# Performance work log

Hardware: AMD Instinct MI355X
Metric: run time of the kernel (lower is better)

The kernel has to match this reference:

```python
import jax, jax.numpy as jnp
import numpy as np

N = 20000      # nodes
E = 256000     # edges
H = 8          # heads
DIN = 256      # in_dim_struct / in_dim_semantic
DH = 32        # num_hidden per head (H*DH == DIN for GT residual)
PRED = 32      # pred_dim (relation embedding dim)
REL = 16       # rel_num
NEG = 0.2      # negative_slope for GAT attention
ALPHA = 0.5    # args.fusion
NUM_LAYERS = 2


def seg_softmax(e, seg, n):
    # softmax over edges grouped by destination node; e: [E, ...], seg: [E]
    m = jax.ops.segment_max(e, seg, num_segments=n)
    ex = jnp.exp(e - m[seg])
    s = jax.ops.segment_sum(ex, seg, num_segments=n)
    return ex / (s[seg] + 1e-9)


def setup_inputs() -> dict:
    key = jax.random.key(0)
    ks = jax.random.split(key, 24)
    f32 = jnp.float32
    def rn(k, shape, scale=0.05):
        return jax.random.normal(k, shape, dtype=f32) * scale
    return {
        "feats_struct": jax.random.normal(ks[0], (N, DIN), f32),
        "feats_semantic": jax.random.normal(ks[1], (N, DIN), f32),
        "centrality": jax.random.uniform(ks[2], (N,), f32),
        # fused per-head scoring MLP (heads[0] small Sequentials batched over H)
        "Ws1": rn(ks[3], (H, DIN, DIN // 2)),
        "bs1": jnp.zeros((H, DIN // 2), f32),
        "Ws2": rn(ks[4], (H, DIN // 2)),
        "bs2": jnp.zeros((H,), f32),
        "rel_emb": rn(ks[5], (REL, PRED), 1.0),
        # SALayer params (2 layers, per-head scalar channels)
        "sa_w": rn(ks[6], (NUM_LAYERS, H), 1.0),
        "sa_al": rn(ks[7], (NUM_LAYERS, H), 1.0),
        "sa_ar": rn(ks[8], (NUM_LAYERS, H), 1.0),
        "sa_We": rn(ks[9], (NUM_LAYERS, PRED, H)),
        # GTLayer params
        "Wq": rn(ks[10], (DIN, H * DH)),
        "bq": jnp.zeros((H * DH,), f32),
        "Wk": rn(ks[11], (DIN, H * DH)),
        "bk": jnp.zeros((H * DH,), f32),
        "Wv": rn(ks[12], (DIN, H * DH)),
        "bv": jnp.zeros((H * DH,), f32),
        "We_gt": rn(ks[13], (PRED, H * DH)),
        "bn_gamma": jnp.ones((H * DH,), f32),
        "bn_beta": jnp.zeros((H * DH,), f32),
        "Wout": rn(ks[14], (H * DH, 1)),
        "bout": jnp.zeros((1,), f32),
        # centrality scale params
        "gamma": jnp.ones((1, H), f32),
        "beta": jnp.zeros((1, H), f32),
        "edge_types": jax.random.randint(ks[15], (E,), 0, REL),
        "edge_src": jax.random.randint(ks[16], (E,), 0, N),
        "edge_dst": jax.random.randint(ks[17], (E,), 0, N),
    }


def _forward(feats_struct, feats_semantic, centrality, Ws1, bs1, Ws2, bs2,
             rel_emb, sa_w, sa_al, sa_ar, sa_We, Wq, bq, Wk, bk, Wv, bv,
             We_gt, bn_gamma, bn_beta, Wout, bout, gamma, beta,
             edge_types, edge_src, edge_dst):
    n = feats_struct.shape[0]
    edge_feats = rel_emb[edge_types]                                   # [E, PRED]

    # ---- structural channel: fused per-head scoring MLPs ----
    h1 = jax.nn.relu(jnp.einsum('nd,hdk->nhk', feats_struct, Ws1) + bs1)  # [N,H,DIN/2]
    h = jnp.einsum('nhk,hk->nh', h1, Ws2) + bs2                           # [N,H]

    # ---- SALayer stack (GAT-style, per-head scalar features) ----
    for l in range(NUM_LAYERS):
        z = h * sa_w[l]                                                 # [N,H]
        e = jax.nn.leaky_relu(z[edge_src] * sa_al[l] + z[edge_dst] * sa_ar[l]
                              + edge_feats @ sa_We[l], NEG)             # [E,H]
        attn = seg_softmax(e, edge_dst, n)                              # [E,H]
        out = jax.ops.segment_sum(attn * z[edge_src], edge_dst, num_segments=n)
        h = jax.nn.elu(out + z)                                         # residual + activation
        if l != NUM_LAYERS - 1:
            h = jnp.mean(h, axis=-1, keepdims=True)
            h = jnp.tile(h, (1, H))
    logits_struct = h                                                   # [N,H]

    # ---- semantic channel: Graph Transformer layer (edge_mode='MUL') ----
    q = (feats_semantic @ Wq + bq).reshape(n, H, DH)
    k = (feats_semantic @ Wk + bk).reshape(n, H, DH)
    v = (feats_semantic @ Wv + bv).reshape(n, H, DH)
    ep = (edge_feats @ We_gt).reshape(-1, H, DH)                        # [E,H,DH]
    ke = k[edge_src] * ep                                               # MUL edge gating
    score = jnp.sum(q[edge_dst] * ke, axis=-1) / jnp.sqrt(jnp.float32(DH))  # [E,H]
    attn = seg_softmax(score, edge_dst, n)                              # [E,H]
    agg = jax.ops.segment_sum(attn[..., None] * v[edge_src], edge_dst,
                              num_segments=n).reshape(n, H * DH)
    agg = agg + feats_semantic                                          # residual (H*DH == DIN)
    mu = jnp.mean(agg, axis=0)
    var = jnp.var(agg, axis=0)
    agg = (agg - mu) / jnp.sqrt(var + 1e-5) * bn_gamma + bn_beta        # batch norm
    h_sem = jax.nn.relu(agg)
    logits_semantic = h_sem @ Wout + bout                               # [N,1]

    # ---- fusion + centrality gamma/beta scaling ----
    logits = ALPHA * logits_struct + (1.0 - ALPHA) * logits_semantic    # [N,H]
    scaled = (centrality[:, None] * gamma + beta) * logits              # [N,H]
    return jax.nn.leaky_relu(jnp.mean(scaled, axis=-1, keepdims=True), 0.01)


def reference(feats_struct, feats_semantic, centrality, Ws1, bs1, Ws2, bs2,
              rel_emb, sa_w, sa_al, sa_ar, sa_We, Wq, bq, Wk, bk, Wv, bv,
              We_gt, bn_gamma, bn_beta, Wout, bout, gamma, beta,
              edge_types, edge_src, edge_dst):
    return _forward(feats_struct, feats_semantic, centrality, Ws1, bs1, Ws2, bs2,
                    rel_emb, sa_w, sa_al, sa_ar, sa_We, Wq, bq, Wk, bk, Wv, bv,
                    We_gt, bn_gamma, bn_beta, Wout, bout, gamma, beta,
                    edge_types, edge_src, edge_dst)
```

## Files before the change

kernel.cpp:

```cpp
#include <hip/hip_runtime.h>
#include <hip/hip_bf16.h>
#include <math.h>

#define N_NODES 20000
#define N_EDGES 256000
#define LOG2E 1.4426950408889634f

typedef __attribute__((ext_vector_type(8))) __bf16 bf16x8;
typedef __attribute__((ext_vector_type(8))) unsigned short u16x8;
typedef __attribute__((ext_vector_type(4))) float f32x4;

static __device__ __forceinline__ unsigned short f2bf(float f) {
  unsigned u = __float_as_uint(f);
  unsigned r = (u + 0x7fffu + ((u >> 16) & 1u)) >> 16;
  return (unsigned short)r;
}
static __device__ __forceinline__ float b2f(unsigned short u) {
  return __uint_as_float((unsigned)u << 16);
}

__global__ __launch_bounds__(256) void k_setup(
    const float* __restrict__ rel_emb, const float* __restrict__ sa_We,
    const float* __restrict__ We_gt, const float* __restrict__ Xs,
    const float* __restrict__ Xm, const float* __restrict__ Ws1,
    const float* __restrict__ Wq, const float* __restrict__ Wk,
    const float* __restrict__ Wv, const int* __restrict__ e_dst,
    float* __restrict__ saTab, float* __restrict__ epTab,
    ushort* __restrict__ Xsb, ushort* __restrict__ Xmb,
    ushort* __restrict__ Ws1t, ushort* __restrict__ Wt,
    int* __restrict__ deg) {
  int b = blockIdx.x;
  int t = threadIdx.x;
  if (b == 0) {
    {
      int l = t >> 7, r = (t >> 3) & 15, h = t & 7;
      float acc = 0.f;
      for (int p = 0; p < 32; ++p)
        acc += rel_emb[r * 32 + p] * sa_We[l * 256 + p * 8 + h];
      saTab[t] = acc * LOG2E;
    }
    for (int r = 0; r < 16; ++r) {
      float acc = 0.f;
      for (int p = 0; p < 32; ++p)
        acc += rel_emb[r * 32 + p] * We_gt[p * 256 + t];
      epTab[r * 256 + t] = acc;
    }
  } else if (b < 5001) {
    size_t i = ((size_t)(b - 1) * 256 + t) * 4;
    float4 a = *(const float4*)(Xs + i);
    ushort4 ua = {f2bf(a.x), f2bf(a.y), f2bf(a.z), f2bf(a.w)};
    *(ushort4*)(Xsb + i) = ua;
    float4 c = *(const float4*)(Xm + i);
    ushort4 uc = {f2bf(c.x), f2bf(c.y), f2bf(c.z), f2bf(c.w)};
    *(ushort4*)(Xmb + i) = uc;
  } else if (b < 6025) {
    int lb = b - 5001;
    int h = lb >> 7, kcol = lb & 127;
    Ws1t[((size_t)h * 128 + kcol) * 256 + t] =
        f2bf(Ws1[((size_t)h * 256 + t) * 128 + kcol]);
  } else if (b < 6793) {
    int lb = b - 6025;
    int m = lb >> 8, n = lb & 255;
    const float* W = (m == 0) ? Wq : (m == 1) ? Wk : Wv;
    Wt[((size_t)m * 256 + n) * 256 + t] = f2bf(W[(size_t)t * 256 + n]);
  } else {
    int e = (b - 6793) * 256 + t;
    if (e < N_EDGES) atomicAdd(&deg[e_dst[e]], 1);
  }
}

__global__ __launch_bounds__(1024) void k_scan(const int* __restrict__ deg,
                                               int* __restrict__ rowPtr,
                                               int* __restrict__ cursor) {
  const int CH = (N_NODES + 1023) / 1024;
  int t = threadIdx.x;
  int b0 = t * CH, b1 = min(b0 + CH, N_NODES);
  int s = 0;
  for (int i = b0; i < b1; ++i) s += deg[i];
  __shared__ int part[1024];
  part[t] = s;
  __syncthreads();
  for (int off = 1; off < 1024; off <<= 1) {
    int add = (t >= off) ? part[t - off] : 0;
    __syncthreads();
    part[t] += add;
    __syncthreads();
  }
  int run = (t == 0) ? 0 : part[t - 1];
  for (int i = b0; i < b1; ++i) {
    rowPtr[i] = run;
    cursor[i] = run;
    run += deg[i];
  }
  if (t == 0) rowPtr[N_NODES] = part[1023];
}

__global__ void k_fill(const int* __restrict__ e_dst, const int* __restrict__ e_src,
                       const int* __restrict__ e_type, int* __restrict__ cursor,
                       int2* __restrict__ csrPack) {
  int e = blockIdx.x * 256 + threadIdx.x;
  if (e >= N_EDGES) return;
  int d = e_dst[e];
  int pos = atomicAdd(&cursor[d], 1);
  csrPack[pos] = make_int2(e_src[e], e_type[e]);
}

__global__ __launch_bounds__(256) void k_gemm(
    const ushort* __restrict__ Xsb, const ushort* __restrict__ Xmb,
    const ushort* __restrict__ Ws1t, const ushort* __restrict__ Wqkvt,
    const float* __restrict__ bs1, const float* __restrict__ Ws2,
    const float* __restrict__ bs2, const float* __restrict__ bq,
    const float* __restrict__ bk, const float* __restrict__ bv,
    float* __restrict__ h0, float* __restrict__ q, ushort* __restrict__ kvB) {
  __shared__ ushort Ab[128][128];
  __shared__ ushort Bb[128][128];
  int tid = threadIdx.x;
  int y = blockIdx.y;
  bool isMlp = (y < 8);
  int m = 0, half = 0;
  const ushort* Bsrc;
  const ushort* Xb;
  if (isMlp) {
    Xb = Xsb;
    Bsrc = Ws1t + (size_t)y * 128 * 256;
  } else {
    m = (y - 8) >> 1;
    half = (y - 8) & 1;
    Xb = Xmb;
    Bsrc = Wqkvt + ((size_t)m * 256 + half * 128) * 256;
  }
  int base = blockIdx.x * 128;
  int wv = tid >> 6, lane = tid & 63;
  int l15 = lane & 15, lhi = lane >> 4;
  int rs = tid >> 4;
  int cs = (tid & 15) * 8;
  f32x4 acc[2][8];
  #pragma unroll
  for (int mr = 0; mr < 2; ++mr)
    #pragma unroll
    for (int nt = 0; nt < 8; ++nt) acc[mr][nt] = (f32x4){0.f, 0.f, 0.f, 0.f};

  for (int kc = 0; kc < 2; ++kc) {
    #pragma unroll
    for (int s = 0; s < 8; ++s) {
      int r = rs + s * 16;
      int csw = cs ^ ((r & 7) << 3);
      int gr = base + r;
      u16x8 val = {0, 0, 0, 0, 0, 0, 0, 0};
      if (gr < N_NODES) val = *(const u16x8*)(Xb + (size_t)gr * 256 + kc * 128 + cs);
      *(u16x8*)&Ab[r][csw] = val;
    }
    #pragma unroll
    for (int s = 0; s < 8; ++s) {
      int r = rs + s * 16;
      int csw = cs ^ ((r & 7) << 3);
      *(u16x8*)&Bb[r][csw] = *(const u16x8*)(Bsrc + (size_t)r * 256 + kc * 128 + cs);
    }
    __syncthreads();
    int swzA = (l15 & 7) << 3;
    #pragma unroll
    for (int kk = 0; kk < 4; ++kk) {
      int col = (kk * 32 + lhi * 8);
      bf16x8 a0 = *(const bf16x8*)&Ab[wv * 32 + l15][col ^ swzA];
      bf16x8 a1 = *(const bf16x8*)&Ab[wv * 32 + 16 + l15][col ^ swzA];
      #pragma unroll
      for (int nt = 0; nt < 8; ++nt) {
        bf16x8 b = *(const bf16x8*)&Bb[nt * 16 + l15][col ^ swzA];
        acc[0][nt] = __builtin_amdgcn_mfma_f32_16x16x32_bf16(a0, b, acc[0][nt], 0, 0, 0);
        acc[1][nt] = __builtin_amdgcn_mfma_f32_16x16x32_bf16(a1, b, acc[1][nt], 0, 0, 0);
      }
    }
    __syncthreads();
  }

  if (isMlp) {
    float part[2][4] = {{0.f, 0.f, 0.f, 0.f}, {0.f, 0.f, 0.f, 0.f}};
    #pragma unroll
    for (int nt = 0; nt < 8; ++nt) {
      int c = y * 128 + nt * 16 + l15;
      float b1 = bs1[c], w2 = Ws2[c];
      #pragma unroll
      for (int mr = 0; mr < 2; ++mr)
        #pragma unroll
        for (int j = 0; j < 4; ++j)
          part[mr][j] += fmaxf(acc[mr][nt][j] + b1, 0.f) * w2;
    }
    #pragma unroll
    for (int mr = 0; mr < 2; ++mr)
      #pragma unroll
      for (int j = 0; j < 4; ++j) {
        #pragma unroll
        for (int o = 1; o < 16; o <<= 1) part[mr][j] += __shfl_xor(part[mr][j], o);
      }
    if (l15 == 0) {
      float b2 = bs2[y];
      #pragma unroll
      for (int mr = 0; mr < 2; ++mr)
        #pragma unroll
        for (int j = 0; j < 4; ++j) {
          int row = base + wv * 32 + mr * 16 + lhi * 4 + j;
          if (row < N_NODES) h0[(size_t)row * 8 + y] = part[mr][j] + b2;
        }
    }
  } else {
    const float* bias = (m == 0) ? bq : (m == 1) ? bk : bv;
    #pragma unroll
    for (int nt = 0; nt < 8; ++nt) {
      int c = half * 128 + nt * 16 + l15;
      float bc = bias[c];
      #pragma unroll
      for (int mr = 0; mr < 2; ++mr)
        #pragma unroll
        for (int j = 0; j < 4; ++j) {
          int row = base + wv * 32 + mr * 16 + lhi * 4 + j;
          if (row < N_NODES) {
            float val = acc[mr][nt][j] + bc;
            if (m == 0) q[(size_t)row * 256 + c] = val;
            else if (m == 1) kvB[(size_t)row * 512 + c] = f2bf(val);
            else kvB[(size_t)row * 512 + 256 + c] = f2bf(val);
          }
        }
    }
  }
}


__global__ __launch_bounds__(256) void k_sa(const float* __restrict__ h_in,
                                            float* __restrict__ h_out,
                                            const int* __restrict__ rowPtr,
                                            const int2* __restrict__ csrPack,
                                            const float* __restrict__ sa_w,
                                            const float* __restrict__ sa_al,
                                            const float* __restrict__ sa_ar,
                                            const float* __restrict__ saTab, int layer) {
  int node = blockIdx.x * 4 + (threadIdx.x >> 6);
  int lane = threadIdx.x & 63;
  int h = lane & 7, eslot = lane >> 3;
  float wgt = sa_w[layer * 8 + h];
  float al2 = sa_al[layer * 8 + h] * LOG2E;
  float ar2 = sa_ar[layer * 8 + h] * LOG2E;
  const float* tab = saTab + layer * 128;
  float zd = h_in[(size_t)node * 8 + h] * wgt;
  int s0 = rowPtr[node], s1 = rowPtr[node + 1];
  float m = -1e30f, lsum = 0.f, acc = 0.f;
  for (int i = s0 + eslot; i < s1; i += 8) {
    int2 p = csrPack[i];
    float zs = h_in[(size_t)p.x * 8 + h] * wgt;
    float e = zs * al2 + zd * ar2 + tab[p.y * 8 + h];
    e = (e >= 0.f) ? e : 0.2f * e;
    float nm = fmaxf(m, e);
    float scl = exp2f(m - nm);
    float pw = exp2f(e - nm);
    acc = acc * scl + pw * zs;
    lsum = lsum * scl + pw;
    m = nm;
  }
  #pragma unroll
  for (int off = 8; off < 64; off <<= 1) {
    float om = __shfl_xor(m, off);
    float ol = __shfl_xor(lsum, off);
    float oa = __shfl_xor(acc, off);
    float nm = fmaxf(m, om);
    float sl = exp2f(m - nm);
    float so = exp2f(om - nm);
    acc = acc * sl + oa * so;
    lsum = lsum * sl + ol * so;
    m = nm;
  }
  float o = acc / (lsum + 1e-9f);
  float r = o + zd;
  r = (r > 0.f) ? r : expm1f(r);
  if (layer == 0) {
    r += __shfl_xor(r, 1);
    r += __shfl_xor(r, 2);
    r += __shfl_xor(r, 4);
    r *= 0.125f;
  }
  if (eslot == 0) h_out[(size_t)node * 8 + h] = r;
}


__global__ __launch_bounds__(256) void k_gt(const float* __restrict__ q,
                                            const ushort* __restrict__ kvB,
                                            const float* __restrict__ epTab,
                                            const float* __restrict__ feats_sem,
                                            const int* __restrict__ rowPtr,
                                            const int2* __restrict__ csrPack,
                                            ushort* __restrict__ agg) {
  int node = blockIdx.x * 4 + (threadIdx.x >> 6);
  int lane = threadIdx.x & 63;
  int c0 = lane * 4;
  const float SC2 = 0.17677669529663687f * LOG2E;
  float4 qv = *(const float4*)(q + (size_t)node * 256 + c0);
  qv.x *= SC2; qv.y *= SC2; qv.z *= SC2; qv.w *= SC2;
  float4 acc = {0.f, 0.f, 0.f, 0.f};
  float m = -1e30f, lsum = 0.f;
  int s0 = rowPtr[node], s1 = rowPtr[node + 1];
  int i = s0;
  for (; i + 1 < s1; i += 2) {
    int2 eA = csrPack[i], eB = csrPack[i + 1];
    const ushort* rA = kvB + (size_t)eA.x * 512 + c0;
    const ushort* rB = kvB + (size_t)eB.x * 512 + c0;
    ushort4 kA = *(const ushort4*)rA;
    ushort4 kB4 = *(const ushort4*)rB;
    float4 epA = *(const float4*)(epTab + eA.y * 256 + c0);
    float4 epB = *(const float4*)(epTab + eB.y * 256 + c0);
    ushort4 vA = *(const ushort4*)(rA + 256);
    ushort4 vB = *(const ushort4*)(rB + 256);
    float pA = qv.x * b2f(kA.x) * epA.x + qv.y * b2f(kA.y) * epA.y +
               qv.z * b2f(kA.z) * epA.z + qv.w * b2f(kA.w) * epA.w;
    float pB = qv.x * b2f(kB4.x) * epB.x + qv.y * b2f(kB4.y) * epB.y +
               qv.z * b2f(kB4.z) * epB.z + qv.w * b2f(kB4.w) * epB.w;
    pA += __shfl_xor(pA, 1); pB += __shfl_xor(pB, 1);
    pA += __shfl_xor(pA, 2); pB += __shfl_xor(pB, 2);
    pA += __shfl_xor(pA, 4); pB += __shfl_xor(pB, 4);
    float nm = fmaxf(m, fmaxf(pA, pB));
    float scl = exp2f(m - nm);
    float wA = exp2f(pA - nm);
    float wB = exp2f(pB - nm);
    acc.x = acc.x * scl + wA * b2f(vA.x) + wB * b2f(vB.x);
    acc.y = acc.y * scl + wA * b2f(vA.y) + wB * b2f(vB.y);
    acc.z = acc.z * scl + wA * b2f(vA.z) + wB * b2f(vB.z);
    acc.w = acc.w * scl + wA * b2f(vA.w) + wB * b2f(vB.w);
    lsum = lsum * scl + wA + wB;
    m = nm;
  }
  if (i < s1) {
    int2 eA = csrPack[i];
    const ushort* rA = kvB + (size_t)eA.x * 512 + c0;
    ushort4 kv = *(const ushort4*)rA;
    float4 ep = *(const float4*)(epTab + eA.y * 256 + c0);
    ushort4 vv = *(const ushort4*)(rA + 256);
    float part = qv.x * b2f(kv.x) * ep.x + qv.y * b2f(kv.y) * ep.y +
                 qv.z * b2f(kv.z) * ep.z + qv.w * b2f(kv.w) * ep.w;
    part += __shfl_xor(part, 1);
    part += __shfl_xor(part, 2);
    part += __shfl_xor(part, 4);
    float nm = fmaxf(m, part);
    float scl = exp2f(m - nm);
    float pw = exp2f(part - nm);
    acc.x = acc.x * scl + pw * b2f(vv.x);
    acc.y = acc.y * scl + pw * b2f(vv.y);
    acc.z = acc.z * scl + pw * b2f(vv.z);
    acc.w = acc.w * scl + pw * b2f(vv.w);
    lsum = lsum * scl + pw;
    m = nm;
  }
  float inv = 1.f / (lsum + 1e-9f);
  float4 fs = *(const float4*)(feats_sem + (size_t)node * 256 + c0);
  ushort4 r;
  r.x = f2bf(acc.x * inv + fs.x);
  r.y = f2bf(acc.y * inv + fs.y);
  r.z = f2bf(acc.z * inv + fs.z);
  r.w = f2bf(acc.w * inv + fs.w);
  *(ushort4*)(agg + (size_t)node * 256 + c0) = r;
}

__global__ void k_bnstats(const ushort* __restrict__ agg, double* __restrict__ colsum,
                          double* __restrict__ colssq) {
  int t = threadIdx.x;
  int r0 = blockIdx.x * 79;
  int r1 = min(r0 + 79, N_NODES);
  double s = 0.0, qq = 0.0;
  for (int r = r0; r < r1; ++r) {
    float x = b2f(agg[(size_t)r * 256 + t]);
    s += (double)x;
    qq += (double)x * (double)x;
  }
  atomicAdd(&colsum[t], s);
  atomicAdd(&colssq[t], qq);
}

__global__ void k_bnfinal(const double* __restrict__ colsum, const double* __restrict__ colssq,
                          float* __restrict__ muArr, float* __restrict__ invArr) {
  int t = threadIdx.x;
  double mu = colsum[t] / (double)N_NODES;
  double var = colssq[t] / (double)N_NODES - mu * mu;
  muArr[t] = (float)mu;
  invArr[t] = (float)(1.0 / sqrt(var + 1e-5));
}

__global__ __launch_bounds__(256) void k_final(const ushort* __restrict__ agg,
                                               const float* __restrict__ muArr,
                                               const float* __restrict__ invArr,
                                               const float* __restrict__ bn_gamma,
                                               const float* __restrict__ bn_beta,
                                               const float* __restrict__ Wout,
                                               const float* __restrict__ bout,
                                               const float* __restrict__ hB,
                                               const float* __restrict__ cent,
                                               const float* __restrict__ gamma,
                                               const float* __restrict__ beta,
                                               float* __restrict__ out) {
  int node = blockIdx.x * 4 + (threadIdx.x >> 6);
  int lane = threadIdx.x & 63;
  int c0 = lane * 4;
  ushort4 xa = *(const ushort4*)(agg + (size_t)node * 256 + c0);
  float4 mu = *(const float4*)(muArr + c0);
  float4 iv = *(const float4*)(invArr + c0);
  float4 g = *(const float4*)(bn_gamma + c0);
  float4 b = *(const float4*)(bn_beta + c0);
  float4 w = *(const float4*)(Wout + c0);
  float p = fmaxf((b2f(xa.x) - mu.x) * iv.x * g.x + b.x, 0.f) * w.x +
            fmaxf((b2f(xa.y) - mu.y) * iv.y * g.y + b.y, 0.f) * w.y +
            fmaxf((b2f(xa.z) - mu.z) * iv.z * g.z + b.z, 0.f) * w.z +
            fmaxf((b2f(xa.w) - mu.w) * iv.w * g.w + b.w, 0.f) * w.w;
  #pragma unroll
  for (int o = 1; o < 64; o <<= 1) p += __shfl_xor(p, o);
  float ls = p + bout[0];
  int h = lane & 7;
  float logit = 0.5f * hB[(size_t)node * 8 + h] + 0.5f * ls;
  float sc = (cent[node] * gamma[h] + beta[h]) * logit;
  sc += __shfl_xor(sc, 1);
  sc += __shfl_xor(sc, 2);
  sc += __shfl_xor(sc, 4);
  float mn = sc * 0.125f;
  mn = (mn >= 0.f) ? mn : 0.01f * mn;
  if (lane == 0) out[node] = mn;
}


extern "C" void kernel_launch(void* const* d_in, const int* in_sizes, int n_in,
                              void* d_out, int out_size, void* d_ws, size_t ws_size,
                              hipStream_t stream) {
  (void)in_sizes; (void)n_in; (void)out_size; (void)ws_size;
  const float* feats_struct = (const float*)d_in[0];
  const float* feats_sem    = (const float*)d_in[1];
  const float* cent         = (const float*)d_in[2];
  const float* Ws1          = (const float*)d_in[3];
  const float* bs1          = (const float*)d_in[4];
  const float* Ws2          = (const float*)d_in[5];
  const float* bs2          = (const float*)d_in[6];
  const float* rel_emb      = (const float*)d_in[7];
  const float* sa_w         = (const float*)d_in[8];
  const float* sa_al        = (const float*)d_in[9];
  const float* sa_ar        = (const float*)d_in[10];
  const float* sa_We        = (const float*)d_in[11];
  const float* Wq           = (const float*)d_in[12];
  const float* bq           = (const float*)d_in[13];
  const float* Wk           = (const float*)d_in[14];
  const float* bk           = (const float*)d_in[15];
  const float* Wv           = (const float*)d_in[16];
  const float* bv           = (const float*)d_in[17];
  const float* We_gt        = (const float*)d_in[18];
  const float* bn_gamma     = (const float*)d_in[19];
  const float* bn_beta      = (const float*)d_in[20];
  const float* Wout         = (const float*)d_in[21];
  const float* bout         = (const float*)d_in[22];
  const float* gamma        = (const float*)d_in[23];
  const float* beta         = (const float*)d_in[24];
  const int* e_type         = (const int*)d_in[25];
  const int* e_src          = (const int*)d_in[26];
  const int* e_dst          = (const int*)d_in[27];
  float* out = (float*)d_out;

  char* wsb = (char*)d_ws;
  size_t off = 0;
  auto alloc = [&](size_t bytes) -> char* {
    char* p = wsb + off;
    off = (off + bytes + 255) & ~(size_t)255;
    return p;
  };
  float* saTab   = (float*)alloc(2 * 16 * 8 * 4);
  float* epTab   = (float*)alloc(16 * 256 * 4);
  int* deg       = (int*)alloc((size_t)N_NODES * 4);
  int* rowPtr    = (int*)alloc((size_t)(N_NODES + 1) * 4);
  int* cursor    = (int*)alloc((size_t)N_NODES * 4);
  int2* csrPack  = (int2*)alloc((size_t)N_EDGES * 8);
  float* h0      = (float*)alloc((size_t)N_NODES * 8 * 4);
  float* hA      = (float*)alloc((size_t)N_NODES * 8 * 4);
  float* hB      = (float*)alloc((size_t)N_NODES * 8 * 4);
  float* qb      = (float*)alloc((size_t)N_NODES * 256 * 4);
  ushort* kvB    = (ushort*)alloc((size_t)N_NODES * 512 * 2);
  ushort* agg    = (ushort*)alloc((size_t)N_NODES * 256 * 2);
  double* colsum = (double*)alloc(256 * 8);
  double* colssq = (double*)alloc(256 * 8);
  float* muArr   = (float*)alloc(256 * 4);
  float* invArr  = (float*)alloc(256 * 4);
  ushort* Xsb    = (ushort*)alloc((size_t)N_NODES * 256 * 2);
  ushort* Xmb    = (ushort*)alloc((size_t)N_NODES * 256 * 2);
  ushort* Ws1t   = (ushort*)alloc((size_t)8 * 128 * 256 * 2);
  ushort* Wqkvt  = (ushort*)alloc((size_t)3 * 256 * 256 * 2);

  hipMemsetAsync(deg, 0, (size_t)N_NODES * 4, stream);
  hipMemsetAsync(colsum, 0, 256 * 8, stream);
  hipMemsetAsync(colssq, 0, 256 * 8, stream);

  k_setup<<<7793, 256, 0, stream>>>(rel_emb, sa_We, We_gt, feats_struct, feats_sem,
                                    Ws1, Wq, Wk, Wv, e_dst,
                                    saTab, epTab, Xsb, Xmb, Ws1t, Wqkvt, deg);
  k_scan<<<1, 1024, 0, stream>>>(deg, rowPtr, cursor);
  k_fill<<<(N_EDGES + 255) / 256, 256, 0, stream>>>(e_dst, e_src, e_type, cursor, csrPack);

  const int MT = (N_NODES + 127) / 128;
  dim3 gGemm(MT, 14);
  k_gemm<<<gGemm, 256, 0, stream>>>(Xsb, Xmb, Ws1t, Wqkvt, bs1, Ws2, bs2,
                                    bq, bk, bv, h0, qb, kvB);
  k_sa<<<(N_NODES + 3) / 4, 256, 0, stream>>>(h0, hA, rowPtr, csrPack,
                                              sa_w, sa_al, sa_ar, saTab, 0);
  k_sa<<<(N_NODES + 3) / 4, 256, 0, stream>>>(hA, hB, rowPtr, csrPack,
                                              sa_w, sa_al, sa_ar, saTab, 1);
  k_gt<<<N_NODES / 4, 256, 0, stream>>>(qb, kvB, epTab, feats_sem,
                                        rowPtr, csrPack, agg);
  k_bnstats<<<256, 256, 0, stream>>>(agg, colsum, colssq);
  k_bnfinal<<<1, 256, 0, stream>>>(colsum, colssq, muArr, invArr);
  k_final<<<N_NODES / 4, 256, 0, stream>>>(agg, muArr, invArr, bn_gamma, bn_beta,
                                           Wout, bout, hB, cent, gamma, beta, out);
}
```

Baseline: 363.9 us.

## Fuse fp32-to-bf16 input conversion into GEMM and keep A tiles in registers

Drops the separate conversion pass that wrote bf16 copies of both feature matrices. The GEMM now loads fp32 rows directly, converts them to bf16 in registers, and holds the full 256-wide A fragment per wave across several output column blocks. B fragments are read straight from global memory instead of LDS, and the grid shrinks from 14 to 4 column groups. This saves a full read/write pass over the inputs and the LDS staging, at the cost of higher register pressure, fewer blocks, and uncoalesced B loads served from cache.

```diff
diff --git a/kernel.cpp b/kernel.cpp
--- a/kernel.cpp
+++ b/kernel.cpp
@@ -21,12 +21,10 @@
 
 __global__ __launch_bounds__(256) void k_setup(
     const float* __restrict__ rel_emb, const float* __restrict__ sa_We,
-    const float* __restrict__ We_gt, const float* __restrict__ Xs,
-    const float* __restrict__ Xm, const float* __restrict__ Ws1,
+    const float* __restrict__ We_gt, const float* __restrict__ Ws1,
     const float* __restrict__ Wq, const float* __restrict__ Wk,
     const float* __restrict__ Wv, const int* __restrict__ e_dst,
     float* __restrict__ saTab, float* __restrict__ epTab,
-    ushort* __restrict__ Xsb, ushort* __restrict__ Xmb,
     ushort* __restrict__ Ws1t, ushort* __restrict__ Wt,
     int* __restrict__ deg) {
   int b = blockIdx.x;
@@ -45,26 +43,18 @@
         acc += rel_emb[r * 32 + p] * We_gt[p * 256 + t];
       epTab[r * 256 + t] = acc;
     }
-  } else if (b < 5001) {
-    size_t i = ((size_t)(b - 1) * 256 + t) * 4;
-    float4 a = *(const float4*)(Xs + i);
-    ushort4 ua = {f2bf(a.x), f2bf(a.y), f2bf(a.z), f2bf(a.w)};
-    *(ushort4*)(Xsb + i) = ua;
-    float4 c = *(const float4*)(Xm + i);
-    ushort4 uc = {f2bf(c.x), f2bf(c.y), f2bf(c.z), f2bf(c.w)};
-    *(ushort4*)(Xmb + i) = uc;
-  } else if (b < 6025) {
-    int lb = b - 5001;
+  } else if (b < 1025) {
+    int lb = b - 1;
     int h = lb >> 7, kcol = lb & 127;
     Ws1t[((size_t)h * 128 + kcol) * 256 + t] =
         f2bf(Ws1[((size_t)h * 256 + t) * 128 + kcol]);
-  } else if (b < 6793) {
-    int lb = b - 6025;
+  } else if (b < 1793) {
+    int lb = b - 1025;
     int m = lb >> 8, n = lb & 255;
     const float* W = (m == 0) ? Wq : (m == 1) ? Wk : Wv;
     Wt[((size_t)m * 256 + n) * 256 + t] = f2bf(W[(size_t)t * 256 + n]);
   } else {
-    int e = (b - 6793) * 256 + t;
+    int e = (b - 1793) * 256 + t;
     if (e < N_EDGES) atomicAdd(&deg[e_dst[e]], 1);
   }
 }
@@ -106,120 +96,134 @@
 }
 
 __global__ __launch_bounds__(256) void k_gemm(
-    const ushort* __restrict__ Xsb, const ushort* __restrict__ Xmb,
+    const float* __restrict__ Xs, const float* __restrict__ Xm,
     const ushort* __restrict__ Ws1t, const ushort* __restrict__ Wqkvt,
     const float* __restrict__ bs1, const float* __restrict__ Ws2,
     const float* __restrict__ bs2, const float* __restrict__ bq,
     const float* __restrict__ bk, const float* __restrict__ bv,
     float* __restrict__ h0, float* __restrict__ q, ushort* __restrict__ kvB) {
-  __shared__ ushort Ab[128][128];
-  __shared__ ushort Bb[128][128];
   int tid = threadIdx.x;
   int y = blockIdx.y;
-  bool isMlp = (y < 8);
-  int m = 0, half = 0;
-  const ushort* Bsrc;
-  const ushort* Xb;
-  if (isMlp) {
-    Xb = Xsb;
-    Bsrc = Ws1t + (size_t)y * 128 * 256;
-  } else {
-    m = (y - 8) >> 1;
-    half = (y - 8) & 1;
-    Xb = Xmb;
-    Bsrc = Wqkvt + ((size_t)m * 256 + half * 128) * 256;
-  }
+  bool isMlp = (y < 2);
   int base = blockIdx.x * 128;
   int wv = tid >> 6, lane = tid & 63;
   int l15 = lane & 15, lhi = lane >> 4;
-  int rs = tid >> 4;
-  int cs = (tid & 15) * 8;
-  f32x4 acc[2][8];
+
+  const float* Xsrc = isMlp ? Xs : Xm;
+  bf16x8 A[2][8];
   #pragma unroll
-  for (int mr = 0; mr < 2; ++mr)
+  for (int mr = 0; mr < 2; ++mr) {
+    int row = base + wv * 32 + mr * 16 + l15;
+    bool ok = row < N_NODES;
+    const float* rp = Xsrc + (size_t)row * 256;
     #pragma unroll
-    for (int nt = 0; nt < 8; ++nt) acc[mr][nt] = (f32x4){0.f, 0.f, 0.f, 0.f};
-
-  for (int kc = 0; kc < 2; ++kc) {
+    for (int kk = 0; kk < 8; ++kk) {
+      float4 x0 = {0.f, 0.f, 0.f, 0.f}, x1 = {0.f, 0.f, 0.f, 0.f};
+      if (ok) {
+        x0 = *(const float4*)(rp + kk * 32 + lhi * 8);
+        x1 = *(const float4*)(rp + kk * 32 + lhi * 8 + 4);
+      }
+      u16x8 tmp;
+      tmp[0] = f2bf(x0.x); tmp[1] = f2bf(x0.y); tmp[2] = f2bf(x0.z); tmp[3] = f2bf(x0.w);
+      tmp[4] = f2bf(x1.x); tmp[5] = f2bf(x1.y); tmp[6] = f2bf(x1.z); tmp[7] = f2bf(x1.w);
+      A[mr][kk] = *(bf16x8*)&tmp;
+    }
+  }
+
+  if (isMlp) {
     #pragma unroll
-    for (int s = 0; s < 8; ++s) {
-      int r = rs + s * 16;
-      int csw = cs ^ ((r & 7) << 3);
-      int gr = base + r;
-      u16x8 val = {0, 0, 0, 0, 0, 0, 0, 0};
-      if (gr < N_NODES) val = *(const u16x8*)(Xb + (size_t)gr * 256 + kc * 128 + cs);
-      *(u16x8*)&Ab[r][csw] = val;
-    }
-    #pragma unroll
-    for (int s = 0; s < 8; ++s) {
-      int r = rs + s * 16;
-      int csw = cs ^ ((r & 7) << 3);
-      *(u16x8*)&Bb[r][csw] = *(const u16x8*)(Bsrc + (size_t)r * 256 + kc * 128 + cs);
-    }
-    __syncthreads();
-    int swzA = (l15 & 7) << 3;
-    #pragma unroll
-    for (int kk = 0; kk < 4; ++kk) {
-      int col = (kk * 32 + lhi * 8);
-      bf16x8 a0 = *(const bf16x8*)&Ab[wv * 32 + l15][col ^ swzA];
-      bf16x8 a1 = *(const bf16x8*)&Ab[wv * 32 + 16 + l15][col ^ swzA];
+    for (int s = 0; s < 4; ++s) {
+      int h = y * 4 + s;
+      const ushort* Bsrc = Ws1t + (size_t)h * 128 * 256;
+      float part[2][4] = {{0.f, 0.f, 0.f, 0.f}, {0.f, 0.f, 0.f, 0.f}};
       #pragma unroll
-      for (int nt = 0; nt < 8; ++nt) {
-        bf16x8 b = *(const bf16x8*)&Bb[nt * 16 + l15][col ^ swzA];
-        acc[0][nt] = __builtin_amdgcn_mfma_f32_16x16x32_bf16(a0, b, acc[0][nt], 0, 0, 0);
-        acc[1][nt] = __builtin_amdgcn_mfma_f32_16x16x32_bf16(a1, b, acc[1][nt], 0, 0, 0);
+      for (int p = 0; p < 2; ++p) {
+        f32x4 acc[2][4];
+        #pragma unroll
+        for (int mr = 0; mr < 2; ++mr)
+          #pragma unroll
+          for (int n4 = 0; n4 < 4; ++n4) acc[mr][n4] = (f32x4){0.f, 0.f, 0.f, 0.f};
+        #pragma unroll
+        for (int kk = 0; kk < 8; ++kk) {
+          #pragma unroll
+          for (int n4 = 0; n4 < 4; ++n4) {
+            int nt = p * 4 + n4;
+            bf16x8 b = *(const bf16x8*)(Bsrc + (size_t)(nt * 16 + l15) * 256 + kk * 32 + lhi * 8);
+            acc[0][n4] = __builtin_amdgcn_mfma_f32_16x16x32_bf16(A[0][kk], b, acc[0][n4], 0, 0, 0);
+            acc[1][n4] = __builtin_amdgcn_mfma_f32_16x16x32_bf16(A[1][kk], b, acc[1][n4], 0, 0, 0);
+          }
+        }
+        #pragma unroll
+        for (int n4 = 0; n4 < 4; ++n4) {
+          int c = h * 128 + (p * 4 + n4) * 16 + l15;
+          float b1 = bs1[c], w2 = Ws2[c];
+          #pragma unroll
+          for (int mr = 0; mr < 2; ++mr)
+            #pragma unroll
+            for (int j = 0; j < 4; ++j)
+              part[mr][j] += fmaxf(acc[mr][n4][j] + b1, 0.f) * w2;
+        }
+      }
+      #pragma unroll
+      for (int mr = 0; mr < 2; ++mr)
+        #pragma unroll
+        for (int j = 0; j < 4; ++j) {
+          #pragma unroll
+          for (int o = 1; o < 16; o <<= 1) part[mr][j] += __shfl_xor(part[mr][j], o);
+        }
+      if (l15 == 0) {
+        float b2 = bs2[h];
+        #pragma unroll
+        for (int mr = 0; mr < 2; ++mr)
+          #pragma unroll
+          for (int j = 0; j < 4; ++j) {
+            int row = base + wv * 32 + mr * 16 + lhi * 4 + j;
+            if (row < N_NODES) h0[(size_t)row * 8 + h] = part[mr][j] + b2;
+          }
       }
     }
-    __syncthreads();
-  }
-
-  if (isMlp) {
-    float part[2][4] = {{0.f, 0.f, 0.f, 0.f}, {0.f, 0.f, 0.f, 0.f}};
+  } else {
     #pragma unroll
-    for (int nt = 0; nt < 8; ++nt) {
-      int c = y * 128 + nt * 16 + l15;
-      float b1 = bs1[c], w2 = Ws2[c];
+    for (int s4 = 0; s4 < 3; ++s4) {
+      int s = (y - 2) * 3 + s4;
+      int m = s >> 1, half = s & 1;
+      const ushort* Bsrc = Wqkvt + ((size_t)m * 256 + half * 128) * 256;
+      const float* bias = (m == 0) ? bq : (m == 1) ? bk : bv;
       #pragma unroll
-      for (int mr = 0; mr < 2; ++mr)
-        #pragma unroll
-        for (int j = 0; j < 4; ++j)
-          part[mr][j] += fmaxf(acc[mr][nt][j] + b1, 0.f) * w2;
-    }
-    #pragma unroll
-    for (int mr = 0; mr < 2; ++mr)
-      #pragma unroll
-      for (int j = 0; j < 4; ++j) {
-        #pragma unroll
-        for (int o = 1; o < 16; o <<= 1) part[mr][j] += __shfl_xor(part[mr][j], o);
-      }
-    if (l15 == 0) {
-      float b2 = bs2[y];
-      #pragma unroll
-      for (int mr = 0; mr < 2; ++mr)
-        #pragma unroll
-        for (int j = 0; j < 4; ++j) {
-          int row = base + wv * 32 + mr * 16 + lhi * 4 + j;
-          if (row < N_NODES) h0[(size_t)row * 8 + y] = part[mr][j] + b2;
-        }
-    }
-  } else {
-    const float* bias = (m == 0) ? bq : (m == 1) ? bk : bv;
-    #pragma unroll
-    for (int nt = 0; nt < 8; ++nt) {
-      int c = half * 128 + nt * 16 + l15;
-      float bc = bias[c];
-      #pragma unroll
-      for (int mr = 0; mr < 2; ++mr)
-        #pragma unroll
-        for (int j = 0; j < 4; ++j) {
-          int row = base + wv * 32 + mr * 16 + lhi * 4 + j;
-          if (row < N_NODES) {
-            float val = acc[mr][nt][j] + bc;
-            if (m == 0) q[(size_t)row * 256 + c] = val;
-            else if (m == 1) kvB[(size_t)row * 512 + c] = f2bf(val);
-            else kvB[(size_t)row * 512 + 256 + c] = f2bf(val);
+      for (int p = 0; p < 2; ++p) {
+        f32x4 acc[2][4];
+        #pragma unroll
+        for (int mr = 0; mr < 2; ++mr)
+          #pragma unroll
+          for (int n4 = 0; n4 < 4; ++n4) acc[mr][n4] = (f32x4){0.f, 0.f, 0.f, 0.f};
+        #pragma unroll
+        for (int kk = 0; kk < 8; ++kk) {
+          #pragma unroll
+          for (int n4 = 0; n4 < 4; ++n4) {
+            int nt = p * 4 + n4;
+            bf16x8 b = *(const bf16x8*)(Bsrc + (size_t)(nt * 16 + l15) * 256 + kk * 32 + lhi * 8);
+            acc[0][n4] = __builtin_amdgcn_mfma_f32_16x16x32_bf16(A[0][kk], b, acc[0][n4], 0, 0, 0);
+            acc[1][n4] = __builtin_amdgcn_mfma_f32_16x16x32_bf16(A[1][kk], b, acc[1][n4], 0, 0, 0);
           }
         }
+        #pragma unroll
+        for (int n4 = 0; n4 < 4; ++n4) {
+          int c = half * 128 + (p * 4 + n4) * 16 + l15;
+          float bc = bias[c];
+          #pragma unroll
+          for (int mr = 0; mr < 2; ++mr)
+            #pragma unroll
+            for (int j = 0; j < 4; ++j) {
+              int row = base + wv * 32 + mr * 16 + lhi * 4 + j;
+              if (row < N_NODES) {
+                float val = acc[mr][n4][j] + bc;
+                if (m == 0) q[(size_t)row * 256 + c] = val;
+                else if (m == 1) kvB[(size_t)row * 512 + c] = f2bf(val);
+                else kvB[(size_t)row * 512 + 256 + c] = f2bf(val);
+              }
+            }
+        }
+      }
     }
   }
 }
@@ -477,8 +481,6 @@
   double* colssq = (double*)alloc(256 * 8);
   float* muArr   = (float*)alloc(256 * 4);
   float* invArr  = (float*)alloc(256 * 4);
-  ushort* Xsb    = (ushort*)alloc((size_t)N_NODES * 256 * 2);
-  ushort* Xmb    = (ushort*)alloc((size_t)N_NODES * 256 * 2);
   ushort* Ws1t   = (ushort*)alloc((size_t)8 * 128 * 256 * 2);
   ushort* Wqkvt  = (ushort*)alloc((size_t)3 * 256 * 256 * 2);
 
@@ -486,16 +488,15 @@
   hipMemsetAsync(colsum, 0, 256 * 8, stream);
   hipMemsetAsync(colssq, 0, 256 * 8, stream);
 
-  k_setup<<<7793, 256, 0, stream>>>(rel_emb, sa_We, We_gt, feats_struct, feats_sem,
-                                    Ws1, Wq, Wk, Wv, e_dst,
-                                    saTab, epTab, Xsb, Xmb, Ws1t, Wqkvt, deg);
+  k_setup<<<2793, 256, 0, stream>>>(rel_emb, sa_We, We_gt, Ws1, Wq, Wk, Wv, e_dst,
+                                    saTab, epTab, Ws1t, Wqkvt, deg);
   k_scan<<<1, 1024, 0, stream>>>(deg, rowPtr, cursor);
   k_fill<<<(N_EDGES + 255) / 256, 256, 0, stream>>>(e_dst, e_src, e_type, cursor, csrPack);
 
   const int MT = (N_NODES + 127) / 128;
-  dim3 gGemm(MT, 14);
-  k_gemm<<<gGemm, 256, 0, stream>>>(Xsb, Xmb, Ws1t, Wqkvt, bs1, Ws2, bs2,
-                                    bq, bk, bv, h0, qb, kvB);
+  dim3 gGemm(MT, 4);
+  k_gemm<<<gGemm, 256, 0, stream>>>(feats_struct, feats_sem, Ws1t, Wqkvt,
+                                    bs1, Ws2, bs2, bq, bk, bv, h0, qb, kvB);
   k_sa<<<(N_NODES + 3) / 4, 256, 0, stream>>>(h0, hA, rowPtr, csrPack,
                                               sa_w, sa_al, sa_ar, saTab, 0);
   k_sa<<<(N_NODES + 3) / 4, 256, 0, stream>>>(hA, hB, rowPtr, csrPack,
```

After: 427.0 us. +17.3%, slower.
